# Kernel optimization log

Hardware: AMD Instinct MI355X
Metric: run time of the kernel (lower is better)

Reference implementation:

```python
import jax, jax.numpy as jnp
import numpy as np

B, NPG, HID, HEADS, L = 8, 512, 128, 8, 4
N = B * NPG
E = 16384
EDIM = HID // 4  # edge_dim = hidden_dim // 4 = 32


def _ln(x, g, b):
    m = x.mean(-1, keepdims=True)
    v = ((x - m) ** 2).mean(-1, keepdims=True)
    return (x - m) / jnp.sqrt(v + 1e-5) * g + b


def setup_inputs() -> dict:
    key = jax.random.key(0)
    ks = jax.random.split(key, 24)
    s = 0.05
    epg = E // B
    base = jnp.repeat(jnp.arange(B) * NPG, epg)
    src = base + jax.random.randint(ks[0], (E,), 0, NPG)
    dst = base + jax.random.randint(ks[1], (E,), 0, NPG)
    d = {
        'x': jax.random.randint(ks[2], (N, 1), 0, 100),
        'edge_index': jnp.stack([src, dst]),
        'edge_attr': jax.random.normal(ks[3], (E, 1), jnp.float32),
        'batch': jnp.repeat(jnp.arange(B), NPG),
        'atom_emb': jax.random.normal(ks[4], (100, HID)) * s,
        'edge_w': jax.random.normal(ks[5], (1, EDIM)) * s,
        'edge_b': jnp.zeros((EDIM,)),
        'wq': jax.random.normal(ks[6], (L, HID, HEADS * HID)) * s,
        'bq': jnp.zeros((L, HEADS * HID)),
        'wk': jax.random.normal(ks[7], (L, HID, HEADS * HID)) * s,
        'bk': jnp.zeros((L, HEADS * HID)),
        'wv': jax.random.normal(ks[8], (L, HID, HEADS * HID)) * s,
        'bv': jnp.zeros((L, HEADS * HID)),
        'we': jax.random.normal(ks[9], (L, EDIM, HEADS * HID)) * s,
        'wskip': jax.random.normal(ks[10], (L, HID, HID)) * s,
        'bskip': jnp.zeros((L, HID)),
        'ln_g': jnp.ones((L, HID)),
        'ln_b': jnp.zeros((L, HID)),
        'mha_in_w': jax.random.normal(ks[11], (HID, 3 * HID)) * s,
        'mha_in_b': jnp.zeros((3 * HID,)),
        'mha_out_w': jax.random.normal(ks[12], (HID, HID)) * s,
        'mha_out_b': jnp.zeros((HID,)),
        'w1': jax.random.normal(ks[13], (HID, HID)) * s,
        'b1': jnp.zeros((HID,)),
        'w2': jax.random.normal(ks[14], (HID, HID // 2)) * s,
        'b2': jnp.zeros((HID // 2,)),
        'w3': jax.random.normal(ks[15], (HID // 2, 3)) * s,
        'b3': jnp.zeros((3,)),
    }
    return d


def reference(x, edge_index, edge_attr, batch, atom_emb, edge_w, edge_b,
              wq, bq, wk, bk, wv, bv, we, wskip, bskip, ln_g, ln_b,
              mha_in_w, mha_in_b, mha_out_w, mha_out_b, w1, b1, w2, b2, w3, b3):
    src, dst = edge_index[0], edge_index[1]
    h = atom_emb[x[:, 0]]                       # [N, HID]
    e = edge_attr @ edge_w + edge_b             # [E, EDIM]
    scale = 1.0 / jnp.sqrt(jnp.float32(HID))    # per-head channel dim = HID
    for i in range(L):
        res = h
        q = (h @ wq[i] + bq[i]).reshape(N, HEADS, HID)
        k = (h @ wk[i] + bk[i]).reshape(N, HEADS, HID)
        v = (h @ wv[i] + bv[i]).reshape(N, HEADS, HID)
        ee = (e @ we[i]).reshape(E, HEADS, HID)
        kj = k[src] + ee                        # [E, HEADS, HID]
        vj = v[src] + ee
        logits = jnp.einsum('ehd,ehd->eh', q[dst], kj) * scale
        m = jax.ops.segment_max(logits, dst, num_segments=N)
        a = jnp.exp(logits - m[dst])
        z = jax.ops.segment_sum(a, dst, num_segments=N)
        a = a / (z[dst] + 1e-16)                # edge softmax per target node
        agg = jax.ops.segment_sum(a[:, :, None] * vj, dst, num_segments=N)
        out = agg.mean(axis=1) + h @ wskip[i] + bskip[i]  # concat=False + root skip
        h = jax.nn.gelu(_ln(out + res, ln_g[i], ln_b[i]), approximate=False)
    # equal-size graphs: ragged->padded conversion is a plain reshape, no padding
    p = h.reshape(B, NPG, HID)
    qkv = p @ mha_in_w + mha_in_b               # [B, n, 3*HID]
    hd = HID // HEADS
    q, k, v = [t.reshape(B, NPG, HEADS, hd).transpose(0, 2, 1, 3)
               for t in jnp.split(qkv, 3, axis=-1)]
    att = jax.nn.softmax(jnp.einsum('bhqd,bhkd->bhqk', q, k) / jnp.sqrt(jnp.float32(hd)), axis=-1)
    o = jnp.einsum('bhqk,bhkd->bhqd', att, v).transpose(0, 2, 1, 3).reshape(B, NPG, HID)
    o = (o @ mha_out_w + mha_out_b).reshape(N, HID)
    y = jax.nn.gelu(o @ w1 + b1, approximate=False)
    y = jax.nn.gelu(y @ w2 + b2, approximate=False)
    return y @ w3 + b3                          # [N, 3]
```

## Files before the change

kernel.cpp:

```cpp
#include <hip/hip_runtime.h>
#include <hip/hip_bf16.h>
#include <math.h>

#define NN 4096
#define NE 16384
#define NLAYERS 4

#define WT_STRIDE 442368

typedef __attribute__((ext_vector_type(8))) short bf16x8;
typedef __attribute__((ext_vector_type(4))) float floatx4;

__device__ __forceinline__ float gelu_f(float x) {
  return 0.5f * x * (1.0f + erff(x * 0.70710678118654752440f));
}

__device__ __forceinline__ void bsplit(float a, unsigned short& hi, unsigned short& lo) {
  __hip_bfloat16 h16 = __float2bfloat16(a);
  hi = *(unsigned short*)&h16;
  const float r = a - __bfloat162float(h16);
  __hip_bfloat16 l16 = __float2bfloat16(r);
  lo = *(unsigned short*)&l16;
}

union F16U { float4 v4[4]; float f[16]; };

__global__ void k_init(const int* __restrict__ x, const float* __restrict__ atom_emb,
                       const float* __restrict__ edge_attr, const float* __restrict__ edge_w,
                       const float* __restrict__ edge_b, float* __restrict__ h,
                       float* __restrict__ ef, int* __restrict__ counts,
                       unsigned short* __restrict__ hhi, unsigned short* __restrict__ hlo) {
  const int idx = blockIdx.x * 256 + threadIdx.x;
  const float hv = atom_emb[x[idx >> 7] * 128 + (idx & 127)];
  h[idx] = hv;
  bsplit(hv, hhi[idx], hlo[idx]);
  ef[idx] = edge_attr[idx >> 5] * edge_w[idx & 31] + edge_b[idx & 31];
  if (idx < NN) counts[idx] = 0;
}

__global__ void k_hist(const int* __restrict__ eidx, int* __restrict__ counts) {
  const int e = blockIdx.x * 256 + threadIdx.x;
  if (e < NE) atomicAdd(&counts[eidx[NE + e]], 1);
}

__global__ void k_scan(const int* __restrict__ counts, int* __restrict__ offs,
                       int* __restrict__ heads) {
  __shared__ int tmp[1024];
  const int t = threadIdx.x;
  const int c0 = counts[t*4], c1 = counts[t*4+1], c2 = counts[t*4+2], c3 = counts[t*4+3];
  const int s = c0 + c1 + c2 + c3;
  tmp[t] = s; __syncthreads();
  for (int off = 1; off < 1024; off <<= 1) {
    int v = (t >= off) ? tmp[t - off] : 0;
    __syncthreads();
    tmp[t] += v;
    __syncthreads();
  }
  int base = tmp[t] - s;
  offs[t*4]   = base;                heads[t*4]   = base;
  offs[t*4+1] = base + c0;           heads[t*4+1] = base + c0;
  offs[t*4+2] = base + c0 + c1;      heads[t*4+2] = base + c0 + c1;
  offs[t*4+3] = base + c0 + c1 + c2; heads[t*4+3] = base + c0 + c1 + c2;
  if (t == 1023) offs[NN] = tmp[1023];
}

__global__ void k_scatter(const int* __restrict__ eidx, int* __restrict__ heads,
                          int* __restrict__ elist) {
  const int e = blockIdx.x * 256 + threadIdx.x;
  if (e < NE) {
    int p = atomicAdd(&heads[eidx[NE + e]], 1);
    elist[p] = e;
  }
}

__global__ __launch_bounds__(256) void k_wcvt(
    const float* __restrict__ wq, const float* __restrict__ wk,
    const float* __restrict__ wv, const float* __restrict__ wsk,
    unsigned short* __restrict__ wthi, unsigned short* __restrict__ wtlo) {
  const int z = blockIdx.z;
  const int layer = z >> 2, mat = z & 3;
  int NC; const float* W; int woff;
  if (mat == 0)      { NC = 1024; W = wq  + (size_t)layer * 131072; woff = 0; }
  else if (mat == 1) { NC = 1024; W = wk  + (size_t)layer * 131072; woff = 131072; }
  else if (mat == 2) { NC = 1024; W = wv  + (size_t)layer * 131072; woff = 262144; }
  else               { NC = 128;  W = wsk + (size_t)layer * 16384;  woff = 393216; }
  const int c0 = blockIdx.x * 64;
  if (c0 >= NC) return;
  const int k0 = blockIdx.y * 64;
  __shared__ unsigned short th[64][65], tl[64][65];
  const int t = threadIdx.x;
  for (int i = t; i < 4096; i += 256) {
    const int kk = i >> 6, c = i & 63;
    bsplit(W[(size_t)(k0 + kk) * NC + c0 + c], th[kk][c], tl[kk][c]);
  }
  __syncthreads();
  unsigned short* oh = wthi + (size_t)layer * WT_STRIDE + woff;
  unsigned short* ol = wtlo + (size_t)layer * WT_STRIDE + woff;
  for (int i = t; i < 4096; i += 256) {
    const int n = i >> 6, k = i & 63;
    oh[(size_t)(c0 + n) * 128 + k0 + k] = th[k][n];
    ol[(size_t)(c0 + n) * 128 + k0 + k] = tl[k][n];
  }
}

__global__ __launch_bounds__(256) void k_wqe(
    const float* __restrict__ wq, const float* __restrict__ bq,
    const float* __restrict__ we, unsigned short* __restrict__ wthi,
    unsigned short* __restrict__ wtlo, float* __restrict__ bqe) {
  const int layer = blockIdx.x >> 3, hh = blockIdx.x & 7;
  const float* wq_l = wq + (size_t)layer * 131072;
  const float* we_l = we + (size_t)layer * 32768;
  const float* bq_l = bq + (size_t)layer * 1024;
  __shared__ float wqS[128][132];
  __shared__ float weS[32][132];
  const int t = threadIdx.x;
  for (int i = t; i < 4096; i += 256) {
    const int d = i >> 5, dd4 = (i & 31) << 2;
    *(float4*)&wqS[d][dd4] = *(const float4*)&wq_l[(size_t)d * 1024 + hh * 128 + dd4];
  }
  for (int i = t; i < 1024; i += 256) {
    const int c = i >> 5, dd4 = (i & 31) << 2;
    *(float4*)&weS[c][dd4] = *(const float4*)&we_l[(size_t)c * 1024 + hh * 128 + dd4];
  }
  __syncthreads();
  const int d = t & 127, cg = t >> 7;
  float acc[16];
  #pragma unroll
  for (int cc = 0; cc < 16; cc++) acc[cc] = 0.f;
  for (int dd = 0; dd < 128; dd++) {
    const float a = wqS[d][dd];
    #pragma unroll
    for (int cc = 0; cc < 16; cc++)
      acc[cc] += a * weS[cg * 16 + cc][dd];
  }
  unsigned short* oh = wthi + (size_t)layer * WT_STRIDE + 409600;
  unsigned short* ol = wtlo + (size_t)layer * WT_STRIDE + 409600;
  #pragma unroll
  for (int cc = 0; cc < 16; cc++) {
    const int j = hh * 32 + cg * 16 + cc;
    unsigned short hi, lo;
    bsplit(acc[cc], hi, lo);
    oh[(size_t)j * 128 + d] = hi;
    ol[(size_t)j * 128 + d] = lo;
  }
  if (t < 32) {
    float s = 0.f;
    for (int dd = 0; dd < 128; dd++) s += bq_l[hh * 128 + dd] * weS[t][dd];
    bqe[layer * 256 + hh * 32 + t] = s;
  }
}

__global__ __launch_bounds__(256) void k_mfqkv(
    const unsigned short* __restrict__ hhi, const unsigned short* __restrict__ hlo,
    const unsigned short* __restrict__ wth, const unsigned short* __restrict__ wtl,
    const float* __restrict__ bq, const float* __restrict__ bk,
    const float* __restrict__ bv, const float* __restrict__ bsk,
    const float* __restrict__ bqe_l,
    float* __restrict__ qb, float* __restrict__ kb,
    float* __restrict__ vb, float* __restrict__ skb, float* __restrict__ qeb) {
  const int xb = blockIdx.x;
  int NC; const float* bias; float* C; int woff; int c0;
  if (xb < 16)      { NC = 1024; bias = bq;    C = qb;  woff = 0;      c0 = xb * 64; }
  else if (xb < 32) { NC = 1024; bias = bk;    C = kb;  woff = 131072; c0 = (xb-16) * 64; }
  else if (xb < 48) { NC = 1024; bias = bv;    C = vb;  woff = 262144; c0 = (xb-32) * 64; }
  else if (xb < 50) { NC = 128;  bias = bsk;   C = skb; woff = 393216; c0 = (xb-48) * 64; }
  else              { NC = 256;  bias = bqe_l; C = qeb; woff = 409600; c0 = (xb-50) * 64; }
  __shared__ unsigned short Ah[64][136], Al[64][136], Wh[64][136], Wl[64][136];
  const int t = threadIdx.x;
  const int n0 = blockIdx.y * 64;
  for (int i = t; i < 1024; i += 256) {
    const int r = i >> 4, c8 = (i & 15) << 3;
    *(uint4*)&Ah[r][c8] = *(const uint4*)&hhi[(size_t)(n0 + r) * 128 + c8];
    *(uint4*)&Al[r][c8] = *(const uint4*)&hlo[(size_t)(n0 + r) * 128 + c8];
    *(uint4*)&Wh[r][c8] = *(const uint4*)&wth[woff + (size_t)(c0 + r) * 128 + c8];
    *(uint4*)&Wl[r][c8] = *(const uint4*)&wtl[woff + (size_t)(c0 + r) * 128 + c8];
  }
  __syncthreads();
  const int w = t >> 6, l = t & 63;
  const int quad = l >> 4, lm = l & 15;
  floatx4 acc[4] = {{0.f,0.f,0.f,0.f},{0.f,0.f,0.f,0.f},{0.f,0.f,0.f,0.f},{0.f,0.f,0.f,0.f}};
  #pragma unroll
  for (int kc = 0; kc < 4; kc++) {
    const int ko = kc * 32 + quad * 8;
    const bf16x8 ah = *(const bf16x8*)&Ah[w * 16 + lm][ko];
    const bf16x8 al = *(const bf16x8*)&Al[w * 16 + lm][ko];
    #pragma unroll
    for (int ct = 0; ct < 4; ct++) {
      const bf16x8 bh = *(const bf16x8*)&Wh[ct * 16 + lm][ko];
      const bf16x8 bl = *(const bf16x8*)&Wl[ct * 16 + lm][ko];
      acc[ct] = __builtin_amdgcn_mfma_f32_16x16x32_bf16(ah, bh, acc[ct], 0, 0, 0);
      acc[ct] = __builtin_amdgcn_mfma_f32_16x16x32_bf16(ah, bl, acc[ct], 0, 0, 0);
      acc[ct] = __builtin_amdgcn_mfma_f32_16x16x32_bf16(al, bh, acc[ct], 0, 0, 0);
    }
  }
  #pragma unroll
  for (int ct = 0; ct < 4; ct++) {
    const int col = c0 + ct * 16 + lm;
    const float bb = bias[col];
    #pragma unroll
    for (int r = 0; r < 4; r++) {
      const int row = n0 + w * 16 + quad * 4 + r;
      C[(size_t)row * NC + col] = acc[ct][r] + bb;
    }
  }
}

__global__ __launch_bounds__(256) void k_gemm2(const float* __restrict__ A,
                                               const float* __restrict__ W,
                                               const float* __restrict__ bias,
                                               float* __restrict__ C, int NC, int gelu) {
  __shared__ float As[128][65];
  __shared__ float Ws[128][64];
  const int t = threadIdx.x;
  const int n0 = blockIdx.y * 64, c0 = blockIdx.x * 64;
  for (int i = t; i < 2048; i += 256) {
    const int r = i & 63, k4 = (i >> 6) << 2;
    const float4 a = *(const float4*)&A[(size_t)(n0 + r) * 128 + k4];
    As[k4+0][r] = a.x; As[k4+1][r] = a.y; As[k4+2][r] = a.z; As[k4+3][r] = a.w;
  }
  for (int i = t; i < 2048; i += 256) {
    const int kk = i >> 4, c4 = (i & 15) << 2;
    *(float4*)&Ws[kk][c4] = *(const float4*)&W[(size_t)kk * NC + c0 + c4];
  }
  __syncthreads();
  const int tr = (t >> 4) << 2;
  const int tc = (t & 15) << 2;
  float acc[4][4];
  #pragma unroll
  for (int i = 0; i < 4; i++)
    #pragma unroll
    for (int j = 0; j < 4; j++) acc[i][j] = 0.f;
  #pragma unroll 8
  for (int k = 0; k < 128; k++) {
    const float4 av = *(const float4*)&As[k][tr];
    const float4 wv = *(const float4*)&Ws[k][tc];
    acc[0][0] += av.x*wv.x; acc[0][1] += av.x*wv.y; acc[0][2] += av.x*wv.z; acc[0][3] += av.x*wv.w;
    acc[1][0] += av.y*wv.x; acc[1][1] += av.y*wv.y; acc[1][2] += av.y*wv.z; acc[1][3] += av.y*wv.w;
    acc[2][0] += av.z*wv.x; acc[2][1] += av.z*wv.y; acc[2][2] += av.z*wv.z; acc[2][3] += av.z*wv.w;
    acc[3][0] += av.w*wv.x; acc[3][1] += av.w*wv.y; acc[3][2] += av.w*wv.z; acc[3][3] += av.w*wv.w;
  }
  const float4 bb = *(const float4*)&bias[c0 + tc];
  #pragma unroll
  for (int i = 0; i < 4; i++) {
    float4 v;
    v.x = acc[i][0] + bb.x; v.y = acc[i][1] + bb.y;
    v.z = acc[i][2] + bb.z; v.w = acc[i][3] + bb.w;
    if (gelu) { v.x = gelu_f(v.x); v.y = gelu_f(v.y); v.z = gelu_f(v.z); v.w = gelu_f(v.w); }
    *(float4*)&C[(size_t)(n0 + tr + i) * NC + c0 + tc] = v;
  }
}

__global__ __launch_bounds__(256) void k_corrpost(
    const float* __restrict__ sbuf, const float* __restrict__ we_l,
    const float* __restrict__ accm, const float* __restrict__ skb,
    const float* __restrict__ lng, const float* __restrict__ lnb,
    float* __restrict__ h,
    unsigned short* __restrict__ hhi, unsigned short* __restrict__ hlo) {
  __shared__ float Ss[8][256];
  __shared__ float sC[8][128];
  const int t = threadIdx.x;
  const int n0 = blockIdx.x * 8;
  for (int i = t; i < 512; i += 256) {
    const int r = i >> 6, c4 = (i & 63) << 2;
    *(float4*)&Ss[r][c4] = *(const float4*)&sbuf[(size_t)(n0 + r) * 256 + c4];
  }
  __syncthreads();
  const int col = t & 127, half = t >> 7;
  float acc[4] = {0.f, 0.f, 0.f, 0.f};
  const float* wp = we_l + col;
  #pragma unroll
  for (int hh = 0; hh < 8; hh++) {
    #pragma unroll 4
    for (int c = 0; c < 32; c++) {
      const float wv = wp[(size_t)c * 1024 + hh * 128];
      const int k = hh * 32 + c;
      #pragma unroll
      for (int j = 0; j < 4; j++)
        acc[j] += Ss[half * 4 + j][k] * wv;
    }
  }
  #pragma unroll
  for (int j = 0; j < 4; j++) {
    const int nn = half * 4 + j;
    const size_t o = (size_t)(n0 + nn) * 128 + col;
    sC[nn][col] = accm[o] + 0.125f * acc[j] + skb[o] + h[o];
  }
  __syncthreads();
  const int g = t >> 5, l = t & 31;
  float v[4];
  #pragma unroll
  for (int jj = 0; jj < 4; jj++) v[jj] = sC[g][l + 32 * jj];
  float s = (v[0] + v[1]) + (v[2] + v[3]);
  #pragma unroll
  for (int mask = 1; mask <= 16; mask <<= 1) s += __shfl_xor(s, mask);
  const float mean = s * (1.f / 128.f);
  float q = 0.f;
  #pragma unroll
  for (int jj = 0; jj < 4; jj++) { const float d = v[jj] - mean; q += d * d; }
  #pragma unroll
  for (int mask = 1; mask <= 16; mask <<= 1) q += __shfl_xor(q, mask);
  const float rstd = 1.f / sqrtf(q * (1.f / 128.f) + 1e-5f);
  #pragma unroll
  for (int jj = 0; jj < 4; jj++) {
    const int c2 = l + 32 * jj;
    const float y = (v[jj] - mean) * rstd * lng[c2] + lnb[c2];
    const float r = gelu_f(y);
    const size_t o = (size_t)(n0 + g) * 128 + c2;
    h[o] = r;
    bsplit(r, hhi[o], hlo[o]);
  }
}

__global__ __launch_bounds__(256) void k_edge(const float* __restrict__ qb,
                                              const float* __restrict__ kb,
                                              const float* __restrict__ vb,
                                              const float* __restrict__ qe,
                                              const float* __restrict__ ef,
                                              const int* __restrict__ offs,
                                              const int* __restrict__ elist,
                                              const int* __restrict__ eidx,
                                              float* __restrict__ accm,
                                              float* __restrict__ sbuf) {
  const int wid = threadIdx.x >> 6;
  const int n = (blockIdx.x & 7) * 512 + (blockIdx.x >> 3) * 4 + wid;
  const int lane = threadIdx.x & 63;
  const int hh = lane >> 3, s8 = lane & 7;
  const int d0 = hh * 128 + s8 * 16;
  F16U qv;
  {
    const float4* qp = (const float4*)(qb + (size_t)n * 1024 + d0);
    #pragma unroll
    for (int i = 0; i < 4; i++) qv.v4[i] = qp[i];
  }
  const float4 qe4 = *(const float4*)(qe + (size_t)n * 256 + hh * 32 + s8 * 4);
  float m = -INFINITY, z = 0.f;
  float acc[16];
  #pragma unroll
  for (int i = 0; i < 16; i++) acc[i] = 0.f;
  float sx = 0.f, sy = 0.f, sz = 0.f, sw = 0.f;
  const int e0 = offs[n], e1 = offs[n + 1];
  for (int tt = e0; tt < e1; tt++) {
    const int e = elist[tt];
    const int src = eidx[e];
    F16U kv;
    {
      const float4* kp = (const float4*)(kb + (size_t)src * 1024 + d0);
      #pragma unroll
      for (int i = 0; i < 4; i++) kv.v4[i] = kp[i];
    }
    const float4 ef4 = *(const float4*)(ef + (size_t)e * 32 + s8 * 4);
    float p0 = qe4.x*ef4.x + qe4.y*ef4.y;
    float p1 = qe4.z*ef4.z + qe4.w*ef4.w;
    float p2 = 0.f, p3 = 0.f;
    #pragma unroll
    for (int i = 0; i < 4; i++) {
      p0 += qv.f[i]      * kv.f[i];
      p1 += qv.f[4 + i]  * kv.f[4 + i];
      p2 += qv.f[8 + i]  * kv.f[8 + i];
      p3 += qv.f[12 + i] * kv.f[12 + i];
    }
    float p = (p0 + p1) + (p2 + p3);
    p += __shfl_xor(p, 1);
    p += __shfl_xor(p, 2);
    p += __shfl_xor(p, 4);
    const float logit = p * 0.08838834764831845f;
    if (logit > m + 8.f) {
      const float f = __expf(m - logit);
      z *= f; sx *= f; sy *= f; sz *= f; sw *= f;
      #pragma unroll
      for (int i = 0; i < 16; i++) acc[i] *= f;
      m = logit;
    }
    const float w = __expf(logit - m);
    z += w;
    F16U vv;
    {
      const float4* vp = (const float4*)(vb + (size_t)src * 1024 + d0);
      #pragma unroll
      for (int i = 0; i < 4; i++) vv.v4[i] = vp[i];
    }
    #pragma unroll
    for (int i = 0; i < 16; i++) acc[i] += w * vv.f[i];
    sx += w * ef4.x; sy += w * ef4.y;
    sz += w * ef4.z; sw += w * ef4.w;
  }
  const float inv = 1.f / (z + 1e-16f);
  *(float4*)(sbuf + (size_t)n * 256 + hh * 32 + s8 * 4) =
      make_float4(sx * inv, sy * inv, sz * inv, sw * inv);
  F16U ov;
  #pragma unroll
  for (int i = 0; i < 16; i++) ov.f[i] = acc[i] * inv;
  #pragma unroll
  for (int mask = 8; mask <= 32; mask <<= 1)
    #pragma unroll
    for (int i = 0; i < 16; i++) ov.f[i] += __shfl_xor(ov.f[i], mask);
  if (hh == 0) {
    #pragma unroll
    for (int i = 0; i < 16; i++) ov.f[i] *= 0.125f;
    float4* ap = (float4*)(accm + (size_t)n * 128 + s8 * 16);
    #pragma unroll
    for (int i = 0; i < 4; i++) ap[i] = ov.v4[i];
  }
}

__global__ __launch_bounds__(256) void k_attn2b(const float* __restrict__ qkvm,
                                                float* __restrict__ pm,
                                                float* __restrict__ pz,
                                                float* __restrict__ pacc) {
  __shared__ float ks2[64][16];
  __shared__ float vs2[64][16];
  const int ksp = blockIdx.x, qt = blockIdx.y, bh = blockIdx.z;
  const int b = bh >> 3, hh = bh & 7;
  const int t = threadIdx.x;
  const size_t rbase = (size_t)(b * 512 + ksp * 64);
  {
    const int j = t >> 2, d4 = (t & 3) << 2;
    const size_t ro = (rbase + j) * 384 + hh * 16 + d4;
    *(float4*)&ks2[j][d4] = *(const float4*)&qkvm[ro + 128];
    *(float4*)&vs2[j][d4] = *(const float4*)&qkvm[ro + 256];
  }
  __syncthreads();
  const int qrow = qt * 256 + t;
  const int nq = b * 512 + qrow;
  F16U qv;
  {
    const float4* qp = (const float4*)(qkvm + (size_t)nq * 384 + hh * 16);
    #pragma unroll
    for (int i = 0; i < 4; i++) qv.v4[i] = qp[i];
  }
  float m = -INFINITY, z = 0.f;
  float acc[16];
  #pragma unroll
  for (int i = 0; i < 16; i++) acc[i] = 0.f;
  for (int j = 0; j < 64; j += 2) {
    F16U k0, k1, v0, v1;
    {
      const float4* p0 = (const float4*)ks2[j];
      const float4* p1 = (const float4*)ks2[j + 1];
      const float4* q0 = (const float4*)vs2[j];
      const float4* q1 = (const float4*)vs2[j + 1];
      #pragma unroll
      for (int i = 0; i < 4; i++) {
        k0.v4[i] = p0[i]; k1.v4[i] = p1[i];
        v0.v4[i] = q0[i]; v1.v4[i] = q1[i];
      }
    }
    float a0 = 0.f, a1 = 0.f, a2 = 0.f, a3 = 0.f;
    float b0 = 0.f, b1 = 0.f, b2 = 0.f, b3 = 0.f;
    #pragma unroll
    for (int i = 0; i < 4; i++) {
      a0 += qv.f[i]      * k0.f[i];
      a1 += qv.f[4 + i]  * k0.f[4 + i];
      a2 += qv.f[8 + i]  * k0.f[8 + i];
      a3 += qv.f[12 + i] * k0.f[12 + i];
      b0 += qv.f[i]      * k1.f[i];
      b1 += qv.f[4 + i]  * k1.f[4 + i];
      b2 += qv.f[8 + i]  * k1.f[8 + i];
      b3 += qv.f[12 + i] * k1.f[12 + i];
    }
    const float sa = ((a0 + a1) + (a2 + a3)) * 0.25f;
    const float sb = ((b0 + b1) + (b2 + b3)) * 0.25f;
    const float smax = fmaxf(sa, sb);
    if (smax > m + 8.f) {
      const float f = __expf(m - smax);
      z *= f;
      #pragma unroll
      for (int i = 0; i < 16; i++) acc[i] *= f;
      m = smax;
    }
    const float wa = __expf(sa - m);
    const float wb = __expf(sb - m);
    z += wa + wb;
    #pragma unroll
    for (int i = 0; i < 16; i++)
      acc[i] += wa * v0.f[i] + wb * v1.f[i];
  }
  const int p = (bh * 512 + qrow) * 8 + ksp;
  pm[p] = m; pz[p] = z;
  float4* pp = (float4*)&pacc[(size_t)p * 16];
  F16U ov;
  #pragma unroll
  for (int i = 0; i < 16; i++) ov.f[i] = acc[i];
  #pragma unroll
  for (int i = 0; i < 4; i++) pp[i] = ov.v4[i];
}

__global__ void k_amerge(const float* __restrict__ pm, const float* __restrict__ pz,
                         const float* __restrict__ pacc, float* __restrict__ ob) {
  const int idx = blockIdx.x * 256 + threadIdx.x;
  if (idx >= 32768) return;
  const int bh = idx >> 9, qrow = idx & 511;
  const int b = bh >> 3, hh = bh & 7;
  float ms = pm[idx*8];
  #pragma unroll
  for (int s = 1; s < 8; s++) ms = fmaxf(ms, pm[idx*8+s]);
  float wgt[8];
  float z = 0.f;
  #pragma unroll
  for (int s = 0; s < 8; s++) {
    wgt[s] = __expf(pm[idx*8+s] - ms);
    z += pz[idx*8+s] * wgt[s];
  }
  const float inv = 1.f / z;
  float* op = &ob[(size_t)(b * 512 + qrow) * 128 + hh * 16];
  #pragma unroll
  for (int d = 0; d < 16; d++) {
    float o = 0.f;
    #pragma unroll
    for (int s = 0; s < 8; s++)
      o += pacc[(size_t)(idx*8+s) * 16 + d] * wgt[s];
    op[d] = o * inv;
  }
}

__global__ void k_final(const float* __restrict__ y2, const float* __restrict__ w3,
                        const float* __restrict__ b3, float* __restrict__ out) {
  const int idx = blockIdx.x * 256 + threadIdx.x;
  if (idx >= NN * 3) return;
  const int n = idx / 3, j = idx % 3;
  float s = b3[j];
  const float* yp = y2 + (size_t)n * 64;
  #pragma unroll
  for (int c = 0; c < 64; c++) s += yp[c] * w3[c * 3 + j];
  out[idx] = s;
}

extern "C" void kernel_launch(void* const* d_in, const int* in_sizes, int n_in,
                              void* d_out, int out_size, void* d_ws, size_t ws_size,
                              hipStream_t stream) {
  const int*   x         = (const int*)d_in[0];
  const int*   eidx      = (const int*)d_in[1];
  const float* edge_attr = (const float*)d_in[2];
  const float* atom_emb  = (const float*)d_in[4];
  const float* edge_w    = (const float*)d_in[5];
  const float* edge_b    = (const float*)d_in[6];
  const float* wq        = (const float*)d_in[7];
  const float* bq        = (const float*)d_in[8];
  const float* wk        = (const float*)d_in[9];
  const float* bk        = (const float*)d_in[10];
  const float* wv        = (const float*)d_in[11];
  const float* bv        = (const float*)d_in[12];
  const float* we        = (const float*)d_in[13];
  const float* wskip     = (const float*)d_in[14];
  const float* bskip     = (const float*)d_in[15];
  const float* ln_g      = (const float*)d_in[16];
  const float* ln_b      = (const float*)d_in[17];
  const float* mha_in_w  = (const float*)d_in[18];
  const float* mha_in_b  = (const float*)d_in[19];
  const float* mha_out_w = (const float*)d_in[20];
  const float* mha_out_b = (const float*)d_in[21];
  const float* w1        = (const float*)d_in[22];
  const float* b1        = (const float*)d_in[23];
  const float* w2        = (const float*)d_in[24];
  const float* b2        = (const float*)d_in[25];
  const float* w3        = (const float*)d_in[26];
  const float* b3        = (const float*)d_in[27];

  float* ws   = (float*)d_ws;
  float* h    = ws;
  float* ef   = h + 524288;
  float* qb   = ef + 524288;
  float* kb   = qb + 4194304;
  float* vb   = kb + 4194304;
  float* qe   = vb + 4194304;
  float* big  = qe + 1048576;
  float* accm = big;
  float* skb  = big + 1048576;
  unsigned short* hhi  = (unsigned short*)(big + 1572864);
  unsigned short* hlo  = hhi + 524288;
  unsigned short* wthi = hlo + 524288;
  unsigned short* wtlo = wthi + 1769472;
  float* sbuf = big + 4194304;
  float* qkvm = qb;
  float* pm   = sbuf;
  float* pz   = sbuf + 262144;
  float* pacc = big;
  float* ob   = kb;
  float* mo   = kb + 524288;
  float* y1   = kb + 1048576;
  float* y2   = kb + 1572864;
  int* counts = (int*)(sbuf + 1048576);
  int* offs   = counts + 4100;
  int* heads  = offs + 4100;
  int* elist  = heads + 4100;
  float* bqe  = (float*)(elist + 16384);

  k_init<<<2048, 256, 0, stream>>>(x, atom_emb, edge_attr, edge_w, edge_b, h, ef, counts,
                                   hhi, hlo);
  k_hist<<<64, 256, 0, stream>>>(eidx, counts);
  k_scan<<<1, 1024, 0, stream>>>(counts, offs, heads);
  k_scatter<<<64, 256, 0, stream>>>(eidx, heads, elist);
  k_wcvt<<<dim3(16, 2, 16), 256, 0, stream>>>(wq, wk, wv, wskip, wthi, wtlo);
  k_wqe<<<32, 256, 0, stream>>>(wq, bq, we, wthi, wtlo, bqe);

  for (int i = 0; i < NLAYERS; i++) {
    const float* bq_i  = bq + (size_t)i * 1024;
    const float* bk_i  = bk + (size_t)i * 1024;
    const float* bv_i  = bv + (size_t)i * 1024;
    const float* we_i  = we + (size_t)i * 32768;
    const float* bsk_i = bskip + (size_t)i * 128;
    const float* g_i   = ln_g + (size_t)i * 128;
    const float* b_i   = ln_b + (size_t)i * 128;
    const unsigned short* wth_i = wthi + (size_t)i * WT_STRIDE;
    const unsigned short* wtl_i = wtlo + (size_t)i * WT_STRIDE;

    k_mfqkv<<<dim3(54, 64), 256, 0, stream>>>(hhi, hlo, wth_i, wtl_i,
                                              bq_i, bk_i, bv_i, bsk_i, bqe + i * 256,
                                              qb, kb, vb, skb, qe);
    k_edge<<<1024, 256, 0, stream>>>(qb, kb, vb, qe, ef, offs, elist, eidx, accm, sbuf);
    k_corrpost<<<512, 256, 0, stream>>>(sbuf, we_i, accm, skb, g_i, b_i, h, hhi, hlo);
  }

  k_gemm2<<<dim3(6, 64), 256, 0, stream>>>(h, mha_in_w, mha_in_b, qkvm, 384, 0);
  k_attn2b<<<dim3(8, 2, 64), 256, 0, stream>>>(qkvm, pm, pz, pacc);
  k_amerge<<<128, 256, 0, stream>>>(pm, pz, pacc, ob);
  k_gemm2<<<dim3(2, 64), 256, 0, stream>>>(ob, mha_out_w, mha_out_b, mo, 128, 0);
  k_gemm2<<<dim3(2, 64), 256, 0, stream>>>(mo, w1, b1, y1, 128, 1);
  k_gemm2<<<dim3(1, 64), 256, 0, stream>>>(y1, w2, b2, y2, 64, 1);
  k_final<<<48, 256, 0, stream>>>(y2, w3, b3, (float*)d_out);
}
```

Measured before the change: 529.6 us.

## Fuse edge attention with post-layer LN and fuse the MLP tail into one kernel

Merges the per-node edge softmax aggregation with the edge-feature correction, residual, LayerNorm and GELU into one kernel of 512 threads handling 8 nodes, keeping intermediates in shared memory rather than global buffers. Also fuses the attention-merge, output projection and the three MLP layers into a single tail kernel per 8 rows. This removes several launches and global round-trips per layer, at the cost of larger blocks and possibly lower occupancy. The tail GEMMs run as scalar FMA loops that re-read the weights from global memory in every block.

```diff
diff --git a/kernel.cpp b/kernel.cpp
--- a/kernel.cpp
+++ b/kernel.cpp
@@ -250,156 +250,142 @@
   }
 }
 
-__global__ __launch_bounds__(256) void k_corrpost(
-    const float* __restrict__ sbuf, const float* __restrict__ we_l,
-    const float* __restrict__ accm, const float* __restrict__ skb,
+__global__ __launch_bounds__(512) void k_edgepost(
+    const float* __restrict__ qb, const float* __restrict__ kb,
+    const float* __restrict__ vb, const float* __restrict__ qe,
+    const float* __restrict__ ef, const int* __restrict__ offs,
+    const int* __restrict__ elist, const int* __restrict__ eidx,
+    const float* __restrict__ we_l, const float* __restrict__ skb,
     const float* __restrict__ lng, const float* __restrict__ lnb,
     float* __restrict__ h,
     unsigned short* __restrict__ hhi, unsigned short* __restrict__ hlo) {
   __shared__ float Ss[8][256];
-  __shared__ float sC[8][128];
-  const int t = threadIdx.x;
-  const int n0 = blockIdx.x * 8;
-  for (int i = t; i < 512; i += 256) {
-    const int r = i >> 6, c4 = (i & 63) << 2;
-    *(float4*)&Ss[r][c4] = *(const float4*)&sbuf[(size_t)(n0 + r) * 256 + c4];
-  }
-  __syncthreads();
-  const int col = t & 127, half = t >> 7;
-  float acc[4] = {0.f, 0.f, 0.f, 0.f};
-  const float* wp = we_l + col;
-  #pragma unroll
-  for (int hh = 0; hh < 8; hh++) {
-    #pragma unroll 4
-    for (int c = 0; c < 32; c++) {
-      const float wv = wp[(size_t)c * 1024 + hh * 128];
-      const int k = hh * 32 + c;
-      #pragma unroll
-      for (int j = 0; j < 4; j++)
-        acc[j] += Ss[half * 4 + j][k] * wv;
-    }
-  }
-  #pragma unroll
-  for (int j = 0; j < 4; j++) {
-    const int nn = half * 4 + j;
-    const size_t o = (size_t)(n0 + nn) * 128 + col;
-    sC[nn][col] = accm[o] + 0.125f * acc[j] + skb[o] + h[o];
-  }
-  __syncthreads();
-  const int g = t >> 5, l = t & 31;
-  float v[4];
-  #pragma unroll
-  for (int jj = 0; jj < 4; jj++) v[jj] = sC[g][l + 32 * jj];
-  float s = (v[0] + v[1]) + (v[2] + v[3]);
-  #pragma unroll
-  for (int mask = 1; mask <= 16; mask <<= 1) s += __shfl_xor(s, mask);
-  const float mean = s * (1.f / 128.f);
-  float q = 0.f;
-  #pragma unroll
-  for (int jj = 0; jj < 4; jj++) { const float d = v[jj] - mean; q += d * d; }
-  #pragma unroll
-  for (int mask = 1; mask <= 16; mask <<= 1) q += __shfl_xor(q, mask);
-  const float rstd = 1.f / sqrtf(q * (1.f / 128.f) + 1e-5f);
-  #pragma unroll
-  for (int jj = 0; jj < 4; jj++) {
-    const int c2 = l + 32 * jj;
-    const float y = (v[jj] - mean) * rstd * lng[c2] + lnb[c2];
-    const float r = gelu_f(y);
-    const size_t o = (size_t)(n0 + g) * 128 + c2;
-    h[o] = r;
-    bsplit(r, hhi[o], hlo[o]);
-  }
-}
-
-__global__ __launch_bounds__(256) void k_edge(const float* __restrict__ qb,
-                                              const float* __restrict__ kb,
-                                              const float* __restrict__ vb,
-                                              const float* __restrict__ qe,
-                                              const float* __restrict__ ef,
-                                              const int* __restrict__ offs,
-                                              const int* __restrict__ elist,
-                                              const int* __restrict__ eidx,
-                                              float* __restrict__ accm,
-                                              float* __restrict__ sbuf) {
-  const int wid = threadIdx.x >> 6;
-  const int n = (blockIdx.x & 7) * 512 + (blockIdx.x >> 3) * 4 + wid;
-  const int lane = threadIdx.x & 63;
-  const int hh = lane >> 3, s8 = lane & 7;
-  const int d0 = hh * 128 + s8 * 16;
-  F16U qv;
-  {
-    const float4* qp = (const float4*)(qb + (size_t)n * 1024 + d0);
-    #pragma unroll
-    for (int i = 0; i < 4; i++) qv.v4[i] = qp[i];
-  }
-  const float4 qe4 = *(const float4*)(qe + (size_t)n * 256 + hh * 32 + s8 * 4);
-  float m = -INFINITY, z = 0.f;
-  float acc[16];
-  #pragma unroll
-  for (int i = 0; i < 16; i++) acc[i] = 0.f;
-  float sx = 0.f, sy = 0.f, sz = 0.f, sw = 0.f;
-  const int e0 = offs[n], e1 = offs[n + 1];
-  for (int tt = e0; tt < e1; tt++) {
-    const int e = elist[tt];
-    const int src = eidx[e];
-    F16U kv;
+  __shared__ float Am[8][128];
+  const int t = threadIdx.x;
+  const int wid = t >> 6, lane = t & 63;
+  const int n0 = (blockIdx.x & 7) * 512 + (blockIdx.x >> 3) * 8;
+  const int n = n0 + wid;
+  {
+    const int hh = lane >> 3, s8 = lane & 7;
+    const int d0 = hh * 128 + s8 * 16;
+    F16U qv;
     {
-      const float4* kp = (const float4*)(kb + (size_t)src * 1024 + d0);
-      #pragma unroll
-      for (int i = 0; i < 4; i++) kv.v4[i] = kp[i];
-    }
-    const float4 ef4 = *(const float4*)(ef + (size_t)e * 32 + s8 * 4);
-    float p0 = qe4.x*ef4.x + qe4.y*ef4.y;
-    float p1 = qe4.z*ef4.z + qe4.w*ef4.w;
-    float p2 = 0.f, p3 = 0.f;
-    #pragma unroll
-    for (int i = 0; i < 4; i++) {
-      p0 += qv.f[i]      * kv.f[i];
-      p1 += qv.f[4 + i]  * kv.f[4 + i];
-      p2 += qv.f[8 + i]  * kv.f[8 + i];
-      p3 += qv.f[12 + i] * kv.f[12 + i];
-    }
-    float p = (p0 + p1) + (p2 + p3);
-    p += __shfl_xor(p, 1);
-    p += __shfl_xor(p, 2);
-    p += __shfl_xor(p, 4);
-    const float logit = p * 0.08838834764831845f;
-    if (logit > m + 8.f) {
-      const float f = __expf(m - logit);
-      z *= f; sx *= f; sy *= f; sz *= f; sw *= f;
-      #pragma unroll
-      for (int i = 0; i < 16; i++) acc[i] *= f;
-      m = logit;
-    }
-    const float w = __expf(logit - m);
-    z += w;
-    F16U vv;
-    {
-      const float4* vp = (const float4*)(vb + (size_t)src * 1024 + d0);
-      #pragma unroll
-      for (int i = 0; i < 4; i++) vv.v4[i] = vp[i];
-    }
-    #pragma unroll
-    for (int i = 0; i < 16; i++) acc[i] += w * vv.f[i];
-    sx += w * ef4.x; sy += w * ef4.y;
-    sz += w * ef4.z; sw += w * ef4.w;
-  }
-  const float inv = 1.f / (z + 1e-16f);
-  *(float4*)(sbuf + (size_t)n * 256 + hh * 32 + s8 * 4) =
-      make_float4(sx * inv, sy * inv, sz * inv, sw * inv);
-  F16U ov;
-  #pragma unroll
-  for (int i = 0; i < 16; i++) ov.f[i] = acc[i] * inv;
-  #pragma unroll
-  for (int mask = 8; mask <= 32; mask <<= 1)
-    #pragma unroll
-    for (int i = 0; i < 16; i++) ov.f[i] += __shfl_xor(ov.f[i], mask);
-  if (hh == 0) {
-    #pragma unroll
-    for (int i = 0; i < 16; i++) ov.f[i] *= 0.125f;
-    float4* ap = (float4*)(accm + (size_t)n * 128 + s8 * 16);
-    #pragma unroll
-    for (int i = 0; i < 4; i++) ap[i] = ov.v4[i];
+      const float4* qp = (const float4*)(qb + (size_t)n * 1024 + d0);
+      #pragma unroll
+      for (int i = 0; i < 4; i++) qv.v4[i] = qp[i];
+    }
+    const float4 qe4 = *(const float4*)(qe + (size_t)n * 256 + hh * 32 + s8 * 4);
+    float m = -INFINITY, z = 0.f;
+    float acc[16];
+    #pragma unroll
+    for (int i = 0; i < 16; i++) acc[i] = 0.f;
+    float sx = 0.f, sy = 0.f, sz = 0.f, sw = 0.f;
+    const int e0 = offs[n], e1 = offs[n + 1];
+    for (int tt = e0; tt < e1; tt++) {
+      const int e = elist[tt];
+      const int src = eidx[e];
+      F16U kv;
+      {
+        const float4* kp = (const float4*)(kb + (size_t)src * 1024 + d0);
+        #pragma unroll
+        for (int i = 0; i < 4; i++) kv.v4[i] = kp[i];
+      }
+      const float4 ef4 = *(const float4*)(ef + (size_t)e * 32 + s8 * 4);
+      float p0 = qe4.x*ef4.x + qe4.y*ef4.y;
+      float p1 = qe4.z*ef4.z + qe4.w*ef4.w;
+      float p2 = 0.f, p3 = 0.f;
+      #pragma unroll
+      for (int i = 0; i < 4; i++) {
+        p0 += qv.f[i]      * kv.f[i];
+        p1 += qv.f[4 + i]  * kv.f[4 + i];
+        p2 += qv.f[8 + i]  * kv.f[8 + i];
+        p3 += qv.f[12 + i] * kv.f[12 + i];
+      }
+      float p = (p0 + p1) + (p2 + p3);
+      p += __shfl_xor(p, 1);
+      p += __shfl_xor(p, 2);
+      p += __shfl_xor(p, 4);
+      const float logit = p * 0.08838834764831845f;
+      if (logit > m + 8.f) {
+        const float f = __expf(m - logit);
+        z *= f; sx *= f; sy *= f; sz *= f; sw *= f;
+        #pragma unroll
+        for (int i = 0; i < 16; i++) acc[i] *= f;
+        m = logit;
+      }
+      const float w = __expf(logit - m);
+      z += w;
+      F16U vv;
+      {
+        const float4* vp = (const float4*)(vb + (size_t)src * 1024 + d0);
+        #pragma unroll
+        for (int i = 0; i < 4; i++) vv.v4[i] = vp[i];
+      }
+      #pragma unroll
+      for (int i = 0; i < 16; i++) acc[i] += w * vv.f[i];
+      sx += w * ef4.x; sy += w * ef4.y;
+      sz += w * ef4.z; sw += w * ef4.w;
+    }
+    const float inv = 1.f / (z + 1e-16f);
+    *(float4*)&Ss[wid][hh * 32 + s8 * 4] =
+        make_float4(sx * inv, sy * inv, sz * inv, sw * inv);
+    F16U ov;
+    #pragma unroll
+    for (int i = 0; i < 16; i++) ov.f[i] = acc[i] * inv;
+    #pragma unroll
+    for (int mask = 8; mask <= 32; mask <<= 1)
+      #pragma unroll
+      for (int i = 0; i < 16; i++) ov.f[i] += __shfl_xor(ov.f[i], mask);
+    if (hh == 0) {
+      #pragma unroll
+      for (int i = 0; i < 16; i++) ov.f[i] *= 0.125f;
+      #pragma unroll
+      for (int i = 0; i < 4; i++)
+        *(float4*)&Am[wid][s8 * 16 + i * 4] = ov.v4[i];
+    }
+  }
+  __syncthreads();
+  {
+    const int col = t & 127, grp = t >> 7;
+    float acc0 = 0.f, acc1 = 0.f;
+    const float* wp = we_l + col;
+    #pragma unroll
+    for (int hh2 = 0; hh2 < 8; hh2++) {
+      #pragma unroll 4
+      for (int c = 0; c < 32; c++) {
+        const float wv = wp[(size_t)c * 1024 + hh2 * 128];
+        const int k = hh2 * 32 + c;
+        acc0 += Ss[grp * 2 + 0][k] * wv;
+        acc1 += Ss[grp * 2 + 1][k] * wv;
+      }
+    }
+    const int nA = grp * 2, nB = grp * 2 + 1;
+    const size_t oA = (size_t)(n0 + nA) * 128 + col;
+    const size_t oB = (size_t)(n0 + nB) * 128 + col;
+    Am[nA][col] = Am[nA][col] + 0.125f * acc0 + skb[oA] + h[oA];
+    Am[nB][col] = Am[nB][col] + 0.125f * acc1 + skb[oB] + h[oB];
+  }
+  __syncthreads();
+  {
+    const float v0 = Am[wid][lane], v1 = Am[wid][lane + 64];
+    float s = v0 + v1;
+    #pragma unroll
+    for (int mask = 1; mask <= 32; mask <<= 1) s += __shfl_xor(s, mask);
+    const float mean = s * (1.f / 128.f);
+    const float d0 = v0 - mean, d1 = v1 - mean;
+    float q = d0 * d0 + d1 * d1;
+    #pragma unroll
+    for (int mask = 1; mask <= 32; mask <<= 1) q += __shfl_xor(q, mask);
+    const float rstd = 1.f / sqrtf(q * (1.f / 128.f) + 1e-5f);
+    const float y0 = d0 * rstd * lng[lane] + lnb[lane];
+    const float y1 = d1 * rstd * lng[lane + 64] + lnb[lane + 64];
+    const float r0 = gelu_f(y0);
+    const float r1 = gelu_f(y1);
+    const size_t o = (size_t)n * 128 + lane;
+    h[o] = r0;
+    h[o + 64] = r1;
+    bsplit(r0, hhi[o], hlo[o]);
+    bsplit(r1, hhi[o + 64], hlo[o + 64]);
   }
 }
 
@@ -485,44 +471,82 @@
   for (int i = 0; i < 4; i++) pp[i] = ov.v4[i];
 }
 
-__global__ void k_amerge(const float* __restrict__ pm, const float* __restrict__ pz,
-                         const float* __restrict__ pacc, float* __restrict__ ob) {
-  const int idx = blockIdx.x * 256 + threadIdx.x;
-  if (idx >= 32768) return;
-  const int bh = idx >> 9, qrow = idx & 511;
-  const int b = bh >> 3, hh = bh & 7;
-  float ms = pm[idx*8];
-  #pragma unroll
-  for (int s = 1; s < 8; s++) ms = fmaxf(ms, pm[idx*8+s]);
-  float wgt[8];
-  float z = 0.f;
-  #pragma unroll
-  for (int s = 0; s < 8; s++) {
-    wgt[s] = __expf(pm[idx*8+s] - ms);
-    z += pz[idx*8+s] * wgt[s];
-  }
-  const float inv = 1.f / z;
-  float* op = &ob[(size_t)(b * 512 + qrow) * 128 + hh * 16];
-  #pragma unroll
-  for (int d = 0; d < 16; d++) {
-    float o = 0.f;
-    #pragma unroll
-    for (int s = 0; s < 8; s++)
-      o += pacc[(size_t)(idx*8+s) * 16 + d] * wgt[s];
-    op[d] = o * inv;
-  }
-}
-
-__global__ void k_final(const float* __restrict__ y2, const float* __restrict__ w3,
-                        const float* __restrict__ b3, float* __restrict__ out) {
-  const int idx = blockIdx.x * 256 + threadIdx.x;
-  if (idx >= NN * 3) return;
-  const int n = idx / 3, j = idx % 3;
-  float s = b3[j];
-  const float* yp = y2 + (size_t)n * 64;
-  #pragma unroll
-  for (int c = 0; c < 64; c++) s += yp[c] * w3[c * 3 + j];
-  out[idx] = s;
+__global__ __launch_bounds__(256) void k_tail(
+    const float* __restrict__ pm, const float* __restrict__ pz,
+    const float* __restrict__ pacc,
+    const float* __restrict__ mha_out_w, const float* __restrict__ mha_out_b,
+    const float* __restrict__ w1, const float* __restrict__ b1,
+    const float* __restrict__ w2, const float* __restrict__ b2,
+    const float* __restrict__ w3, const float* __restrict__ b3,
+    float* __restrict__ out) {
+  __shared__ float R0[8][128];
+  __shared__ float R1[8][128];
+  const int t = threadIdx.x;
+  const int n0 = blockIdx.x * 8;
+  for (int i = t; i < 1024; i += 256) {
+    const int r = i >> 7, c = i & 127;
+    const int n = n0 + r, b = n >> 9, qrow = n & 511;
+    const int hh = c >> 4, d = c & 15;
+    const int base = ((b * 8 + hh) * 512 + qrow) * 8;
+    float ms = pm[base];
+    #pragma unroll
+    for (int s = 1; s < 8; s++) ms = fmaxf(ms, pm[base + s]);
+    float z = 0.f, o = 0.f;
+    #pragma unroll
+    for (int s = 0; s < 8; s++) {
+      const float w = __expf(pm[base + s] - ms);
+      z += pz[base + s] * w;
+      o += pacc[(size_t)(base + s) * 16 + d] * w;
+    }
+    R0[r][c] = o / z;
+  }
+  __syncthreads();
+  {
+    const int c = t & 127, rg = t >> 7;
+    float a0 = 0.f, a1 = 0.f, a2 = 0.f, a3 = 0.f;
+    #pragma unroll 4
+    for (int k = 0; k < 128; k++) {
+      const float wv = mha_out_w[k * 128 + c];
+      a0 += R0[rg*4+0][k] * wv; a1 += R0[rg*4+1][k] * wv;
+      a2 += R0[rg*4+2][k] * wv; a3 += R0[rg*4+3][k] * wv;
+    }
+    const float bb = mha_out_b[c];
+    R1[rg*4+0][c] = a0 + bb; R1[rg*4+1][c] = a1 + bb;
+    R1[rg*4+2][c] = a2 + bb; R1[rg*4+3][c] = a3 + bb;
+  }
+  __syncthreads();
+  {
+    const int c = t & 127, rg = t >> 7;
+    float a0 = 0.f, a1 = 0.f, a2 = 0.f, a3 = 0.f;
+    #pragma unroll 4
+    for (int k = 0; k < 128; k++) {
+      const float wv = w1[k * 128 + c];
+      a0 += R1[rg*4+0][k] * wv; a1 += R1[rg*4+1][k] * wv;
+      a2 += R1[rg*4+2][k] * wv; a3 += R1[rg*4+3][k] * wv;
+    }
+    const float bb = b1[c];
+    R0[rg*4+0][c] = gelu_f(a0 + bb); R0[rg*4+1][c] = gelu_f(a1 + bb);
+    R0[rg*4+2][c] = gelu_f(a2 + bb); R0[rg*4+3][c] = gelu_f(a3 + bb);
+  }
+  __syncthreads();
+  {
+    const int c = t & 63, rg = t >> 6;
+    float a0 = 0.f, a1 = 0.f;
+    #pragma unroll 4
+    for (int k = 0; k < 128; k++) {
+      const float wv = w2[k * 64 + c];
+      a0 += R0[rg*2+0][k] * wv; a1 += R0[rg*2+1][k] * wv;
+    }
+    const float bb = b2[c];
+    R1[rg*2+0][c] = gelu_f(a0 + bb); R1[rg*2+1][c] = gelu_f(a1 + bb);
+  }
+  __syncthreads();
+  if (t < 24) {
+    const int r = t / 3, j = t % 3;
+    float s = b3[j];
+    for (int c = 0; c < 64; c++) s += R1[r][c] * w3[c * 3 + j];
+    out[(size_t)(n0 + r) * 3 + j] = s;
+  }
 }
 
 extern "C" void kernel_launch(void* const* d_in, const int* in_sizes, int n_in,
@@ -564,7 +588,6 @@
   float* vb   = kb + 4194304;
   float* qe   = vb + 4194304;
   float* big  = qe + 1048576;
-  float* accm = big;
   float* skb  = big + 1048576;
   unsigned short* hhi  = (unsigned short*)(big + 1572864);
   unsigned short* hlo  = hhi + 524288;
@@ -575,10 +598,6 @@
   float* pm   = sbuf;
   float* pz   = sbuf + 262144;
   float* pacc = big;
-  float* ob   = kb;
-  float* mo   = kb + 524288;
-  float* y1   = kb + 1048576;
-  float* y2   = kb + 1572864;
   int* counts = (int*)(sbuf + 1048576);
   int* offs   = counts + 4100;
   int* heads  = offs + 4100;
@@ -607,15 +626,13 @@
     k_mfqkv<<<dim3(54, 64), 256, 0, stream>>>(hhi, hlo, wth_i, wtl_i,
                                               bq_i, bk_i, bv_i, bsk_i, bqe + i * 256,
                                               qb, kb, vb, skb, qe);
-    k_edge<<<1024, 256, 0, stream>>>(qb, kb, vb, qe, ef, offs, elist, eidx, accm, sbuf);
-    k_corrpost<<<512, 256, 0, stream>>>(sbuf, we_i, accm, skb, g_i, b_i, h, hhi, hlo);
+    k_edgepost<<<512, 512, 0, stream>>>(qb, kb, vb, qe, ef, offs, elist, eidx,
+                                        we_i, skb, g_i, b_i, h, hhi, hlo);
   }
 
   k_gemm2<<<dim3(6, 64), 256, 0, stream>>>(h, mha_in_w, mha_in_b, qkvm, 384, 0);
   k_attn2b<<<dim3(8, 2, 64), 256, 0, stream>>>(qkvm, pm, pz, pacc);
-  k_amerge<<<128, 256, 0, stream>>>(pm, pz, pacc, ob);
-  k_gemm2<<<dim3(2, 64), 256, 0, stream>>>(ob, mha_out_w, mha_out_b, mo, 128, 0);
-  k_gemm2<<<dim3(2, 64), 256, 0, stream>>>(mo, w1, b1, y1, 128, 1);
-  k_gemm2<<<dim3(1, 64), 256, 0, stream>>>(y1, w2, b2, y2, 64, 1);
-  k_final<<<48, 256, 0, stream>>>(y2, w3, b3, (float*)d_out);
-}
+  k_tail<<<512, 256, 0, stream>>>(pm, pz, pacc,
+                                  mha_out_w, mha_out_b, w1, b1, w2, b2, w3, b3,
+                                  (float*)d_out);
+}
```

Result: faster. 480.0 us (-9.4%).
